# Kernel optimization log

Hardware: AMD Instinct MI355X
Metric: run time of the kernel (lower is better)

The kernel has to match this reference:

```python
import jax, jax.numpy as jnp
import numpy as np

# Dims: batch, in-ch, out-ch, deform kernel, channels-per-offset-group, input H/W
B, CIN, COUT, K, CPG, H, W = 16, 64, 64, 3, 8, 130, 130
G = CIN // CPG                 # number of deformable offset groups = 8
HO, WO = H - 2, W - 2          # conv1 (3x3, VALID) output == deform-conv output (3x3, VALID)
DN = ('NCHW', 'OIHW', 'NCHW')


def _conv(x, w, b):
    y = jax.lax.conv_general_dilated(x, w, (1, 1), 'VALID', dimension_numbers=DN)
    return y + b[None, :, None, None]


def setup_inputs() -> dict:
    key = jax.random.key(0)
    k0, k1, k2, k3 = jax.random.split(key, 4)
    def wn(k, shape, fan_in, scale=1.0):
        return jax.random.normal(k, shape, jnp.float32) * (scale / np.sqrt(fan_in))
    return {
        'x':  jax.random.normal(k0, (B, CIN, H, W), jnp.float32),
        'w1': wn(k1, (CIN, CIN, 3, 3), CIN * 9),
        'b1': jnp.zeros((CIN,), jnp.float32),
        # small scale so predicted offsets stay in a realistic sub-pixel/pixel range
        'w2': wn(k2, (G * 2 * K * K, CIN, 1, 1), CIN, scale=0.1),
        'b2': jnp.zeros((G * 2 * K * K,), jnp.float32),
        'wd': wn(k3, (COUT, CIN, K, K), CIN * K * K),
    }


def _deform_conv(x, off, wd):
    # x: [B,CIN,H,W], off: [B,G*2*K*K,HO,WO], wd: [COUT,CIN,K,K]
    Bq, Cin, Hx, Wx = x.shape
    offr = off.reshape(Bq, G, K, K, 2, HO, WO)     # (dy, dx) per group/kernel-pos/pixel
    xg = x.reshape(Bq, G, CPG, Hx * Wx)            # grouped input, flat spatial
    hh = jnp.arange(HO, dtype=x.dtype)[:, None]
    ww = jnp.arange(WO, dtype=x.dtype)[None, :]
    out = jnp.zeros((Bq, COUT, HO, WO), x.dtype)

    def gather(yi, xi, valid):
        # yi/xi: clipped int coords [B,G,HO,WO]; valid: 0/1 mask (zero padding outside)
        idx = (yi * Wx + xi).reshape(Bq, G, 1, HO * WO)
        v = jnp.take_along_axis(xg, jnp.broadcast_to(idx, (Bq, G, CPG, HO * WO)), axis=-1)
        return v.reshape(Bq, G, CPG, HO, WO) * valid[:, :, None, :, :]

    for i in range(K):
        for j in range(K):
            py = offr[:, :, i, j, 0] + (hh + i)    # [B,G,HO,WO] sample row (float)
            px = offr[:, :, i, j, 1] + (ww + j)    # [B,G,HO,WO] sample col (float)
            y0 = jnp.floor(py); x0 = jnp.floor(px)
            ly = py - y0;       lx = px - x0
            y0i = y0.astype(jnp.int32); x0i = x0.astype(jnp.int32)
            y1i = y0i + 1;              x1i = x0i + 1
            inb = lambda yi, xi: ((yi >= 0) & (yi < Hx) & (xi >= 0) & (xi < Wx)).astype(x.dtype)
            yc0 = jnp.clip(y0i, 0, Hx - 1); yc1 = jnp.clip(y1i, 0, Hx - 1)
            xc0 = jnp.clip(x0i, 0, Wx - 1); xc1 = jnp.clip(x1i, 0, Wx - 1)
            v = (((1 - ly) * (1 - lx))[:, :, None] * gather(yc0, xc0, inb(y0i, x0i))
               + ((1 - ly) * lx)[:, :, None]       * gather(yc0, xc1, inb(y0i, x1i))
               + (ly * (1 - lx))[:, :, None]       * gather(yc1, xc0, inb(y1i, x0i))
               + (ly * lx)[:, :, None]             * gather(yc1, xc1, inb(y1i, x1i)))
            # accumulate this kernel tap: v [B,G,CPG,HO,WO] x wd[:,:,i,j] [COUT,G,CPG]
            out = out + jnp.einsum('bgchw,ogc->bohw', v, wd[:, :, i, j].reshape(COUT, G, CPG))
    return out


def reference(x, w1, b1, w2, b2, wd):
    off = _conv(_conv(x, w1, b1), w2, b2)          # [B, G*2*K*K, HO, WO]
    y = _deform_conv(x, off, wd)                   # [B, COUT, HO, WO]
    return (y, off)
```

## Files before the change

### kernel.cpp

```cpp
#include <hip/hip_runtime.h>

typedef unsigned short u16;
typedef unsigned int u32;
typedef __attribute__((ext_vector_type(8))) short bfrag;
typedef __attribute__((ext_vector_type(4))) float ffrag;

constexpr int B_ = 16, CIN = 64, COUT = 64, G = 8, CPG = 8;
constexpr int H = 130, W = 130, HO = 128, WO = 128;
constexpr int OFFC = 144;
constexpr int PLANE_IN = H * W;
constexpr int PLANE_OUT = HO * WO;

constexpr size_t WB1_BYTE = 36864 * 4;
constexpr size_t WB2_BYTE = WB1_BYTE + 36864 * 2;
constexpr size_t XT_BYTE  = 262144;
constexpr size_t XT_SIZE  = (size_t)B_ * PLANE_IN * 64 * 2;

__device__ __forceinline__ u16 f2bf(float f) {
    union { u32 u; float f; } t; t.f = f;
    return (u16)((t.u + 0x7FFFu + ((t.u >> 16) & 1u)) >> 16);
}
__device__ __forceinline__ float bf2f(short h) {
    union { u32 u; float f; } t; t.u = ((u32)(u16)h) << 16;
    return t.f;
}

__global__ void prep_weights(const float* __restrict__ w1,
                             const float* __restrict__ wd,
                             const float* __restrict__ w2,
                             float* __restrict__ wsf) {
    u16* wdB = (u16*)wsf;
    u16* wB1 = (u16*)((char*)wsf + WB1_BYTE);
    u16* wB2 = (u16*)((char*)wsf + WB2_BYTE);
    int idx = blockIdx.x * 256 + threadIdx.x;
    if (idx < 36864) {
        int co = idx / 576, r = idx % 576;
        int t = r >> 6, ci = r & 63;
        wdB[idx] = f2bf(wd[(co * 64 + ci) * 9 + t]);
    } else if (idx < 73728) {
        int j = idx - 36864;
        int co = j / 576, r = j % 576;
        int t = r >> 6, ci = r & 63;
        wB1[j] = f2bf(w1[(co * 64 + ci) * 9 + t]);
    } else if (idx < 82944) {
        int j = idx - 73728;
        wB2[j] = f2bf(w2[j]);
    }
}

__global__ __launch_bounds__(256) void x_to_nhwc(const float* __restrict__ x,
                                                 u16* __restrict__ xt) {
    int p = blockIdx.x * 256 + threadIdx.x;
    if (p >= B_ * PLANE_IN) return;
    int b = p / PLANE_IN, pp = p % PLANE_IN;
    const float* xb = x + (size_t)b * CIN * PLANE_IN + pp;
    u16* dst = xt + (size_t)p * 64;
    #pragma unroll
    for (int oct = 0; oct < 8; ++oct) {
        union { u16 h[8]; uint4 q; } pk;
        #pragma unroll
        for (int j = 0; j < 8; ++j)
            pk.h[j] = f2bf(xb[(size_t)(oct * 8 + j) * PLANE_IN]);
        *(uint4*)(dst + oct * 8) = pk.q;
    }
}

union ConvSmem {
    char xsb[324 * 128];
    char hsb[4][64 * 128];
};
__device__ __forceinline__ int swz128(int row, int bytecol) {
    return row * 128 + (bytecol ^ ((row & 7) << 4));
}

template<bool XT>
__global__ __launch_bounds__(256) void conv12(const float* __restrict__ x,
                                              const u16* __restrict__ xt,
                                              const float* __restrict__ b1,
                                              const float* __restrict__ b2,
                                              const float* __restrict__ wsf,
                                              float* __restrict__ off_out) {
    __shared__ ConvSmem sm;
    const u16* wB1 = (const u16*)((const char*)wsf + WB1_BYTE);
    const u16* wB2 = (const u16*)((const char*)wsf + WB2_BYTE);
    const int b = blockIdx.z;
    const int y0 = blockIdx.y * 16, x0 = blockIdx.x * 16;
    const int tid = threadIdx.x;
    const int wave = tid >> 6, lane = tid & 63;
    const int n16 = lane & 15, quad = lane >> 4;

    if constexpr (XT) {
        const u16* xtb = xt + (size_t)b * PLANE_IN * 64;
        for (int idx = tid; idx < 324 * 8; idx += 256) {
            int p = idx >> 3, oct = idx & 7;
            *(bfrag*)(sm.xsb + swz128(p, oct * 16)) =
                *(const bfrag*)&xtb[((size_t)(y0 + p / 18) * W + x0 + p % 18) * 64 + oct * 8];
        }
    } else {
        const float* xb = x + (size_t)b * CIN * PLANE_IN;
        for (int idx = tid; idx < 324 * 64; idx += 256) {
            int ci = idx / 324, p = idx % 324;
            float v = xb[(size_t)ci * PLANE_IN + (y0 + p / 18) * W + (x0 + p % 18)];
            *(u16*)(sm.xsb + swz128(p, ci * 2)) = f2bf(v);
        }
    }
    __syncthreads();

    ffrag acc[4][4];
    #pragma unroll
    for (int nt = 0; nt < 4; ++nt) {
        float bv = b1[nt * 16 + n16];
        #pragma unroll
        for (int mt = 0; mt < 4; ++mt) acc[mt][nt] = ffrag{bv, bv, bv, bv};
    }

    #pragma unroll
    for (int s = 0; s < 18; ++s) {
        const int tap = s >> 1, cib = (s & 1) * 32;
        const int ti = tap / 3, tj = tap % 3;
        bfrag a[4], bb[4];
        #pragma unroll
        for (int mt = 0; mt < 4; ++mt) {
            int p = (wave * 4 + mt + ti) * 18 + n16 + tj;
            a[mt] = *(const bfrag*)(sm.xsb + swz128(p, cib * 2 + quad * 16));
        }
        #pragma unroll
        for (int nt = 0; nt < 4; ++nt)
            bb[nt] = *(const bfrag*)&wB1[(nt * 16 + n16) * 576 + tap * 64 + cib + quad * 8];
        #pragma unroll
        for (int mt = 0; mt < 4; ++mt)
            #pragma unroll
            for (int nt = 0; nt < 4; ++nt)
                acc[mt][nt] = __builtin_amdgcn_mfma_f32_16x16x32_bf16(
                    a[mt], bb[nt], acc[mt][nt], 0, 0, 0);
    }

    __syncthreads();

    #pragma unroll
    for (int mt = 0; mt < 4; ++mt)
        #pragma unroll
        for (int nt = 0; nt < 4; ++nt)
            #pragma unroll
            for (int r = 0; r < 4; ++r)
                *(u16*)(sm.hsb[wave] + swz128(mt * 16 + quad * 4 + r, (nt * 16 + n16) * 2))
                    = f2bf(acc[mt][nt][r]);
    __syncthreads();

    bfrag a2[4][2];
    #pragma unroll
    for (int mt = 0; mt < 4; ++mt)
        #pragma unroll
        for (int s2 = 0; s2 < 2; ++s2)
            a2[mt][s2] = *(const bfrag*)(sm.hsb[wave]
                        + swz128(mt * 16 + n16, s2 * 64 + quad * 16));

    float* offb = off_out + (size_t)b * OFFC * PLANE_OUT;
    #pragma unroll 1
    for (int nt2 = 0; nt2 < 9; ++nt2) {
        bfrag b2f[2];
        #pragma unroll
        for (int s2 = 0; s2 < 2; ++s2)
            b2f[s2] = *(const bfrag*)&wB2[(nt2 * 16 + n16) * 64 + s2 * 32 + quad * 8];
        float bv = b2[nt2 * 16 + n16];
        #pragma unroll
        for (int mt = 0; mt < 4; ++mt) {
            ffrag acc2 = ffrag{bv, bv, bv, bv};
            acc2 = __builtin_amdgcn_mfma_f32_16x16x32_bf16(a2[mt][0], b2f[0], acc2, 0, 0, 0);
            acc2 = __builtin_amdgcn_mfma_f32_16x16x32_bf16(a2[mt][1], b2f[1], acc2, 0, 0, 0);
            float* dst = offb + (size_t)(nt2 * 16 + n16) * PLANE_OUT
                       + (y0 + wave * 4 + mt) * WO + x0 + quad * 4;
            *(ffrag*)dst = acc2;
        }
    }
}

__device__ __forceinline__ bfrag interp1(bfrag q0, bfrag q1, bfrag q2, bfrag q3,
                                         float w0, float w1, float w2, float w3) {
    union { u16 h[8]; bfrag f; } pk;
    #pragma unroll
    for (int j = 0; j < 8; ++j) {
        float v = w0 * bf2f(q0[j]) + w1 * bf2f(q1[j])
                + w2 * bf2f(q2[j]) + w3 * bf2f(q3[j]);
        pk.h[j] = f2bf(v);
    }
    return pk.f;
}

constexpr int TR = 14, TC = 22, TILE_PX = TR * TC;

__device__ __forceinline__ bfrag lds_px(const char* xls, int p, int g) {
    return *(const bfrag*)(xls + p * 128 + ((g * 16) ^ ((p & 7) << 4)));
}

template<bool XT>
__global__ __launch_bounds__(256, 4) void deform_k(const float* __restrict__ x,
                                                   const u16* __restrict__ xt,
                                                   const float* __restrict__ wsf,
                                                   const float* __restrict__ off_in,
                                                   float* __restrict__ y_out) {
    __shared__ char xls[TILE_PX * 128];
    const u16* wdB = (const u16*)wsf;

    const int wg = blockIdx.x;
    const int swz = (wg & 7) * 256 + (wg >> 3);
    const int b = swz >> 7, sp = swz & 127;
    const int y0 = (sp >> 3) * 8, x0 = (sp & 7) * 16;
    const int ylo = y0 - 2, xlo = x0 - 2;

    const int tid = threadIdx.x;
    const int wave = tid >> 6, lane = tid & 63;
    const int n16 = lane & 15, quad = lane >> 4;
    const int wo = x0 + n16;

    const float* offbase = off_in + (size_t)b * OFFC * PLANE_OUT + x0 + n16;
    const u16* xtb = xt + (size_t)b * PLANE_IN * 64;
    const float* xb = x + (size_t)b * CIN * PLANE_IN;

    if constexpr (XT) {
        for (int idx = tid; idx < TILE_PX * 8; idx += 256) {
            int oct = idx & 7, pix = idx >> 3;
            int ty = pix / TC, tx = pix % TC;
            int iy = min(max(ylo + ty, 0), H - 1);
            int ix = min(max(xlo + tx, 0), W - 1);
            *(bfrag*)(xls + pix * 128 + ((oct * 16) ^ ((pix & 7) << 4)))
                = *(const bfrag*)&xtb[((size_t)(iy * W + ix)) * 64 + oct * 8];
        }
        __syncthreads();
    }

    ffrag acc[2][4];
    #pragma unroll
    for (int mt = 0; mt < 2; ++mt)
        #pragma unroll
        for (int nt = 0; nt < 4; ++nt) acc[mt][nt] = ffrag{0.f, 0.f, 0.f, 0.f};

    float pdy[4], pdx[4];
    #pragma unroll
    for (int tk = 0; tk < 4; ++tk) {
        const int mt = tk >> 1, g = quad + (tk & 1) * 4;
        const float* ob = offbase + (y0 + wave * 2 + mt) * WO
                        + (size_t)(g * 9 * 2) * PLANE_OUT;
        pdy[tk] = ob[0];
        pdx[tk] = ob[PLANE_OUT];
    }

    #pragma unroll 1
    for (int t = 0; t < 9; ++t) {
        const int ki = t / 3, kj = t % 3;

        float dyv[4], dxv[4];
        #pragma unroll
        for (int tk = 0; tk < 4; ++tk) { dyv[tk] = pdy[tk]; dxv[tk] = pdx[tk]; }

        if (t < 8) {
            #pragma unroll
            for (int tk = 0; tk < 4; ++tk) {
                const int mt = tk >> 1, g = quad + (tk & 1) * 4;
                const float* ob = offbase + (y0 + wave * 2 + mt) * WO
                                + (size_t)((g * 9 + t + 1) * 2) * PLANE_OUT;
                pdy[tk] = ob[0];
                pdx[tk] = ob[PLANE_OUT];
            }
        }

        #pragma unroll
        for (int half = 0; half < 2; ++half) {
            const int g = quad + half * 4;
            bfrag bw0 = *(const bfrag*)&wdB[(size_t)(0 * 16 + n16) * 576 + t * 64 + half * 32 + quad * 8];
            bfrag bw1 = *(const bfrag*)&wdB[(size_t)(1 * 16 + n16) * 576 + t * 64 + half * 32 + quad * 8];
            bfrag bw2 = *(const bfrag*)&wdB[(size_t)(2 * 16 + n16) * 576 + t * 64 + half * 32 + quad * 8];
            bfrag bw3 = *(const bfrag*)&wdB[(size_t)(3 * 16 + n16) * 576 + t * 64 + half * 32 + quad * 8];

            #pragma unroll
            for (int mt = 0; mt < 2; ++mt) {
                const int tk = mt * 2 + half;
                const int ho = y0 + wave * 2 + mt;
                float py = dyv[tk] + (float)(ho + ki);
                float px = dxv[tk] + (float)(wo + kj);
                float y0f = floorf(py), x0f = floorf(px);
                float ly = py - y0f, lx = px - x0f;
                int yi0 = (int)y0f, xi0 = (int)x0f;
                int yi1 = yi0 + 1, xi1 = xi0 + 1;
                float vy0 = (yi0 >= 0 && yi0 < H) ? 1.f : 0.f;
                float vy1 = (yi1 >= 0 && yi1 < H) ? 1.f : 0.f;
                float vx0 = (xi0 >= 0 && xi0 < W) ? 1.f : 0.f;
                float vx1 = (xi1 >= 0 && xi1 < W) ? 1.f : 0.f;
                float w00 = (1.f - ly) * (1.f - lx) * vy0 * vx0;
                float w01 = (1.f - ly) * lx         * vy0 * vx1;
                float w10 = ly * (1.f - lx)         * vy1 * vx0;
                float w11 = ly * lx                 * vy1 * vx1;
                int yc0 = min(max(yi0, 0), H - 1), yc1 = min(max(yi1, 0), H - 1);
                int xc0 = min(max(xi0, 0), W - 1), xc1 = min(max(xi1, 0), W - 1);

                bfrag q00, q01, q10, q11;
                if constexpr (XT) {
                    int ry0 = yc0 - ylo, ry1 = yc1 - ylo;
                    int rx0 = xc0 - xlo, rx1 = xc1 - xlo;
                    bool intile = ((u32)ry0 < TR) & ((u32)ry1 < TR)
                                & ((u32)rx0 < TC) & ((u32)rx1 < TC);
                    if (intile) {
                        q00 = lds_px(xls, ry0 * TC + rx0, g);
                        q01 = lds_px(xls, ry0 * TC + rx1, g);
                        q10 = lds_px(xls, ry1 * TC + rx0, g);
                        q11 = lds_px(xls, ry1 * TC + rx1, g);
                    } else {
                        q00 = *(const bfrag*)&xtb[(size_t)(yc0 * W + xc0) * 64 + g * 8];
                        q01 = *(const bfrag*)&xtb[(size_t)(yc0 * W + xc1) * 64 + g * 8];
                        q10 = *(const bfrag*)&xtb[(size_t)(yc1 * W + xc0) * 64 + g * 8];
                        q11 = *(const bfrag*)&xtb[(size_t)(yc1 * W + xc1) * 64 + g * 8];
                    }
                } else {
                    int i00 = yc0 * W + xc0, i01 = yc0 * W + xc1;
                    int i10 = yc1 * W + xc0, i11 = yc1 * W + xc1;
                    const float* xg = xb + (size_t)g * CPG * PLANE_IN;
                    union { u16 h[8]; bfrag f; } p00, p01, p10, p11;
                    #pragma unroll
                    for (int cc = 0; cc < 8; ++cc) {
                        const float* xp = xg + cc * PLANE_IN;
                        p00.h[cc] = f2bf(xp[i00]); p01.h[cc] = f2bf(xp[i01]);
                        p10.h[cc] = f2bf(xp[i10]); p11.h[cc] = f2bf(xp[i11]);
                    }
                    q00 = p00.f; q01 = p01.f; q10 = p10.f; q11 = p11.f;
                }

                bfrag fr = interp1(q00, q01, q10, q11, w00, w01, w10, w11);

                acc[mt][0] = __builtin_amdgcn_mfma_f32_16x16x32_bf16(fr, bw0, acc[mt][0], 0, 0, 0);
                acc[mt][1] = __builtin_amdgcn_mfma_f32_16x16x32_bf16(fr, bw1, acc[mt][1], 0, 0, 0);
                acc[mt][2] = __builtin_amdgcn_mfma_f32_16x16x32_bf16(fr, bw2, acc[mt][2], 0, 0, 0);
                acc[mt][3] = __builtin_amdgcn_mfma_f32_16x16x32_bf16(fr, bw3, acc[mt][3], 0, 0, 0);
            }
        }
    }

    float* yb = y_out + (size_t)b * COUT * PLANE_OUT;
    #pragma unroll
    for (int nt = 0; nt < 4; ++nt)
        #pragma unroll
        for (int mt = 0; mt < 2; ++mt) {
            float* dst = yb + (size_t)(nt * 16 + n16) * PLANE_OUT
                       + (y0 + wave * 2 + mt) * WO + x0 + quad * 4;
            *(ffrag*)dst = acc[mt][nt];
        }
}

extern "C" void kernel_launch(void* const* d_in, const int* in_sizes, int n_in,
                              void* d_out, int out_size, void* d_ws, size_t ws_size,
                              hipStream_t stream) {
    const float* x  = (const float*)d_in[0];
    const float* w1 = (const float*)d_in[1];
    const float* b1 = (const float*)d_in[2];
    const float* w2 = (const float*)d_in[3];
    const float* b2 = (const float*)d_in[4];
    const float* wd = (const float*)d_in[5];
    float* y_out = (float*)d_out;
    float* off_out = y_out + (size_t)B_ * COUT * PLANE_OUT;
    float* wsf = (float*)d_ws;
    u16* xt = (u16*)((char*)d_ws + XT_BYTE);
    const bool use_xt = ws_size >= XT_BYTE + XT_SIZE;

    prep_weights<<<324, 256, 0, stream>>>(w1, wd, w2, wsf);
    if (use_xt) {
        x_to_nhwc<<<(B_ * PLANE_IN + 255) / 256, 256, 0, stream>>>(x, xt);
        conv12<true><<<dim3(8, 8, B_), 256, 0, stream>>>(x, xt, b1, b2, wsf, off_out);
        deform_k<true><<<2048, 256, 0, stream>>>(x, xt, wsf, off_out, y_out);
    } else {
        conv12<false><<<dim3(8, 8, B_), 256, 0, stream>>>(x, xt, b1, b2, wsf, off_out);
        deform_k<false><<<2048, 256, 0, stream>>>(x, xt, wsf, off_out, y_out);
    }
}
```

Before: 431.4 us.

## Prefetch conv weights one step ahead and shrink deform input halo tile

In conv12, the first-stage and second-stage weight fragments are now loaded one iteration ahead in registers. The main K loop is no longer unrolled, and the kernel gets a launch-bounds occupancy hint. In deform_k, the staged input tile shrinks from a 2-pixel halo to a 1-pixel halo, which cuts LDS per block, and the occupancy hint rises to 5 blocks per CU. This trades possible extra fallback gathers for samples that land outside the smaller tile, and looser unrolling, for more resident waves and hidden weight-load latency.

```diff
diff --git a/kernel.cpp b/kernel.cpp
--- a/kernel.cpp
+++ b/kernel.cpp
@@ -74,12 +74,12 @@
 }
 
 template<bool XT>
-__global__ __launch_bounds__(256) void conv12(const float* __restrict__ x,
-                                              const u16* __restrict__ xt,
-                                              const float* __restrict__ b1,
-                                              const float* __restrict__ b2,
-                                              const float* __restrict__ wsf,
-                                              float* __restrict__ off_out) {
+__global__ __launch_bounds__(256, 3) void conv12(const float* __restrict__ x,
+                                                 const u16* __restrict__ xt,
+                                                 const float* __restrict__ b1,
+                                                 const float* __restrict__ b2,
+                                                 const float* __restrict__ wsf,
+                                                 float* __restrict__ off_out) {
     __shared__ ConvSmem sm;
     const u16* wB1 = (const u16*)((const char*)wsf + WB1_BYTE);
     const u16* wB2 = (const u16*)((const char*)wsf + WB2_BYTE);
@@ -114,25 +114,37 @@
         for (int mt = 0; mt < 4; ++mt) acc[mt][nt] = ffrag{bv, bv, bv, bv};
     }
 
-    #pragma unroll
+    bfrag nb0 = *(const bfrag*)&wB1[(0 * 16 + n16) * 576 + quad * 8];
+    bfrag nb1 = *(const bfrag*)&wB1[(1 * 16 + n16) * 576 + quad * 8];
+    bfrag nb2 = *(const bfrag*)&wB1[(2 * 16 + n16) * 576 + quad * 8];
+    bfrag nb3 = *(const bfrag*)&wB1[(3 * 16 + n16) * 576 + quad * 8];
+
+    #pragma unroll 1
     for (int s = 0; s < 18; ++s) {
         const int tap = s >> 1, cib = (s & 1) * 32;
         const int ti = tap / 3, tj = tap % 3;
-        bfrag a[4], bb[4];
+        bfrag bb0 = nb0, bb1 = nb1, bb2 = nb2, bb3 = nb3;
+        if (s < 17) {
+            const int s2 = s + 1;
+            const int koff = (s2 >> 1) * 64 + (s2 & 1) * 32 + quad * 8;
+            nb0 = *(const bfrag*)&wB1[(0 * 16 + n16) * 576 + koff];
+            nb1 = *(const bfrag*)&wB1[(1 * 16 + n16) * 576 + koff];
+            nb2 = *(const bfrag*)&wB1[(2 * 16 + n16) * 576 + koff];
+            nb3 = *(const bfrag*)&wB1[(3 * 16 + n16) * 576 + koff];
+        }
+        bfrag a[4];
         #pragma unroll
         for (int mt = 0; mt < 4; ++mt) {
             int p = (wave * 4 + mt + ti) * 18 + n16 + tj;
             a[mt] = *(const bfrag*)(sm.xsb + swz128(p, cib * 2 + quad * 16));
         }
         #pragma unroll
-        for (int nt = 0; nt < 4; ++nt)
-            bb[nt] = *(const bfrag*)&wB1[(nt * 16 + n16) * 576 + tap * 64 + cib + quad * 8];
-        #pragma unroll
-        for (int mt = 0; mt < 4; ++mt)
-            #pragma unroll
-            for (int nt = 0; nt < 4; ++nt)
-                acc[mt][nt] = __builtin_amdgcn_mfma_f32_16x16x32_bf16(
-                    a[mt], bb[nt], acc[mt][nt], 0, 0, 0);
+        for (int mt = 0; mt < 4; ++mt) {
+            acc[mt][0] = __builtin_amdgcn_mfma_f32_16x16x32_bf16(a[mt], bb0, acc[mt][0], 0, 0, 0);
+            acc[mt][1] = __builtin_amdgcn_mfma_f32_16x16x32_bf16(a[mt], bb1, acc[mt][1], 0, 0, 0);
+            acc[mt][2] = __builtin_amdgcn_mfma_f32_16x16x32_bf16(a[mt], bb2, acc[mt][2], 0, 0, 0);
+            acc[mt][3] = __builtin_amdgcn_mfma_f32_16x16x32_bf16(a[mt], bb3, acc[mt][3], 0, 0, 0);
+        }
     }
 
     __syncthreads();
@@ -156,18 +168,22 @@
                         + swz128(mt * 16 + n16, s2 * 64 + quad * 16));
 
     float* offb = off_out + (size_t)b * OFFC * PLANE_OUT;
+    bfrag c0n = *(const bfrag*)&wB2[(size_t)n16 * 64 + quad * 8];
+    bfrag c1n = *(const bfrag*)&wB2[(size_t)n16 * 64 + 32 + quad * 8];
     #pragma unroll 1
     for (int nt2 = 0; nt2 < 9; ++nt2) {
-        bfrag b2f[2];
-        #pragma unroll
-        for (int s2 = 0; s2 < 2; ++s2)
-            b2f[s2] = *(const bfrag*)&wB2[(nt2 * 16 + n16) * 64 + s2 * 32 + quad * 8];
+        bfrag b2f0 = c0n, b2f1 = c1n;
+        if (nt2 < 8) {
+            const u16* wp = &wB2[(size_t)((nt2 + 1) * 16 + n16) * 64 + quad * 8];
+            c0n = *(const bfrag*)wp;
+            c1n = *(const bfrag*)(wp + 32);
+        }
         float bv = b2[nt2 * 16 + n16];
         #pragma unroll
         for (int mt = 0; mt < 4; ++mt) {
             ffrag acc2 = ffrag{bv, bv, bv, bv};
-            acc2 = __builtin_amdgcn_mfma_f32_16x16x32_bf16(a2[mt][0], b2f[0], acc2, 0, 0, 0);
-            acc2 = __builtin_amdgcn_mfma_f32_16x16x32_bf16(a2[mt][1], b2f[1], acc2, 0, 0, 0);
+            acc2 = __builtin_amdgcn_mfma_f32_16x16x32_bf16(a2[mt][0], b2f0, acc2, 0, 0, 0);
+            acc2 = __builtin_amdgcn_mfma_f32_16x16x32_bf16(a2[mt][1], b2f1, acc2, 0, 0, 0);
             float* dst = offb + (size_t)(nt2 * 16 + n16) * PLANE_OUT
                        + (y0 + wave * 4 + mt) * WO + x0 + quad * 4;
             *(ffrag*)dst = acc2;
@@ -187,14 +203,14 @@
     return pk.f;
 }
 
-constexpr int TR = 14, TC = 22, TILE_PX = TR * TC;
+constexpr int TR = 12, TC = 20, TILE_PX = TR * TC;
 
 __device__ __forceinline__ bfrag lds_px(const char* xls, int p, int g) {
     return *(const bfrag*)(xls + p * 128 + ((g * 16) ^ ((p & 7) << 4)));
 }
 
 template<bool XT>
-__global__ __launch_bounds__(256, 4) void deform_k(const float* __restrict__ x,
+__global__ __launch_bounds__(256, 5) void deform_k(const float* __restrict__ x,
                                                    const u16* __restrict__ xt,
                                                    const float* __restrict__ wsf,
                                                    const float* __restrict__ off_in,
@@ -206,7 +222,7 @@
     const int swz = (wg & 7) * 256 + (wg >> 3);
     const int b = swz >> 7, sp = swz & 127;
     const int y0 = (sp >> 3) * 8, x0 = (sp & 7) * 16;
-    const int ylo = y0 - 2, xlo = x0 - 2;
+    const int ylo = y0 - 1, xlo = x0 - 1;
 
     const int tid = threadIdx.x;
     const int wave = tid >> 6, lane = tid & 63;
```

Result: slower. 583.4 us (+35.2%).

## Fuse offset convolutions and deformable conv into one kernel per tile

Applied to the files above, without the earlier changes.

Merges the conv1+conv2 offset kernel and the deformable conv kernel into a single fused kernel over 16x16 tiles. It loads a 20x20 halo tile of NHWC bf16 input into LDS once and reuses it for both the 3x3 conv and the bilinear gathers. Offsets are written to global and read back in the same block, removing one launch and the duplicated tile load. The cost is far fewer blocks (1024 vs 2048), a larger per-thread register footprint with launch bounds lowered to 2, and a per-row barrier loop in the second conv stage. The fallback non-NHWC path is kept as separate simplified kernels.

```diff
diff --git a/kernel.cpp b/kernel.cpp
--- a/kernel.cpp
+++ b/kernel.cpp
@@ -65,44 +65,53 @@
     }
 }
 
-union ConvSmem {
-    char xsb[324 * 128];
-    char hsb[4][64 * 128];
-};
 __device__ __forceinline__ int swz128(int row, int bytecol) {
     return row * 128 + (bytecol ^ ((row & 7) << 4));
 }
-
-template<bool XT>
-__global__ __launch_bounds__(256) void conv12(const float* __restrict__ x,
-                                              const u16* __restrict__ xt,
-                                              const float* __restrict__ b1,
-                                              const float* __restrict__ b2,
-                                              const float* __restrict__ wsf,
-                                              float* __restrict__ off_out) {
-    __shared__ ConvSmem sm;
+__device__ __forceinline__ bfrag lds_px(const char* xls, int p, int g) {
+    return *(const bfrag*)(xls + p * 128 + ((g * 16) ^ ((p & 7) << 4)));
+}
+__device__ __forceinline__ bfrag interp1(bfrag q0, bfrag q1, bfrag q2, bfrag q3,
+                                         float w0, float w1, float w2, float w3) {
+    union { u16 h[8]; bfrag f; } pk;
+    #pragma unroll
+    for (int j = 0; j < 8; ++j) {
+        float v = w0 * bf2f(q0[j]) + w1 * bf2f(q1[j])
+                + w2 * bf2f(q2[j]) + w3 * bf2f(q3[j]);
+        pk.h[j] = f2bf(v);
+    }
+    return pk.f;
+}
+
+constexpr int FTR = 20, FTC = 20, FT_PX = FTR * FTC;
+
+__global__ __launch_bounds__(256, 2) void fused_cd(const u16* __restrict__ xt,
+                                                   const float* __restrict__ b1,
+                                                   const float* __restrict__ b2,
+                                                   const float* __restrict__ wsf,
+                                                   float* __restrict__ off_out,
+                                                   float* __restrict__ y_out) {
+    __shared__ char xls[FT_PX * 128];
+    __shared__ char hsl[4][16 * 128];
+    const u16* wdB = (const u16*)wsf;
     const u16* wB1 = (const u16*)((const char*)wsf + WB1_BYTE);
     const u16* wB2 = (const u16*)((const char*)wsf + WB2_BYTE);
+
     const int b = blockIdx.z;
     const int y0 = blockIdx.y * 16, x0 = blockIdx.x * 16;
+    const int ylo = y0 - 1, xlo = x0 - 1;
     const int tid = threadIdx.x;
     const int wave = tid >> 6, lane = tid & 63;
     const int n16 = lane & 15, quad = lane >> 4;
-
-    if constexpr (XT) {
-        const u16* xtb = xt + (size_t)b * PLANE_IN * 64;
-        for (int idx = tid; idx < 324 * 8; idx += 256) {
-            int p = idx >> 3, oct = idx & 7;
-            *(bfrag*)(sm.xsb + swz128(p, oct * 16)) =
-                *(const bfrag*)&xtb[((size_t)(y0 + p / 18) * W + x0 + p % 18) * 64 + oct * 8];
-        }
-    } else {
-        const float* xb = x + (size_t)b * CIN * PLANE_IN;
-        for (int idx = tid; idx < 324 * 64; idx += 256) {
-            int ci = idx / 324, p = idx % 324;
-            float v = xb[(size_t)ci * PLANE_IN + (y0 + p / 18) * W + (x0 + p % 18)];
-            *(u16*)(sm.xsb + swz128(p, ci * 2)) = f2bf(v);
-        }
+    const u16* xtb = xt + (size_t)b * PLANE_IN * 64;
+
+    for (int idx = tid; idx < FT_PX * 8; idx += 256) {
+        int oct = idx & 7, pix = idx >> 3;
+        int ty = pix / FTC, tx = pix % FTC;
+        int iy = min(max(ylo + ty, 0), H - 1);
+        int ix = min(max(xlo + tx, 0), W - 1);
+        *(bfrag*)(xls + pix * 128 + ((oct * 16) ^ ((pix & 7) << 4)))
+            = *(const bfrag*)&xtb[((size_t)(iy * W + ix)) * 64 + oct * 8];
     }
     __syncthreads();
 
@@ -113,7 +122,6 @@
         #pragma unroll
         for (int mt = 0; mt < 4; ++mt) acc[mt][nt] = ffrag{bv, bv, bv, bv};
     }
-
     #pragma unroll
     for (int s = 0; s < 18; ++s) {
         const int tap = s >> 1, cib = (s & 1) * 32;
@@ -121,8 +129,8 @@
         bfrag a[4], bb[4];
         #pragma unroll
         for (int mt = 0; mt < 4; ++mt) {
-            int p = (wave * 4 + mt + ti) * 18 + n16 + tj;
-            a[mt] = *(const bfrag*)(sm.xsb + swz128(p, cib * 2 + quad * 16));
+            int p = (wave * 4 + mt + ti + 1) * FTC + (n16 + tj + 1);
+            a[mt] = *(const bfrag*)(xls + swz128(p, cib * 2 + quad * 16));
         }
         #pragma unroll
         for (int nt = 0; nt < 4; ++nt)
@@ -135,149 +143,72 @@
                     a[mt], bb[nt], acc[mt][nt], 0, 0, 0);
     }
 
-    __syncthreads();
-
-    #pragma unroll
-    for (int mt = 0; mt < 4; ++mt)
-        #pragma unroll
-        for (int nt = 0; nt < 4; ++nt)
-            #pragma unroll
-            for (int r = 0; r < 4; ++r)
-                *(u16*)(sm.hsb[wave] + swz128(mt * 16 + quad * 4 + r, (nt * 16 + n16) * 2))
-                    = f2bf(acc[mt][nt][r]);
-    __syncthreads();
-
-    bfrag a2[4][2];
-    #pragma unroll
-    for (int mt = 0; mt < 4; ++mt)
-        #pragma unroll
-        for (int s2 = 0; s2 < 2; ++s2)
-            a2[mt][s2] = *(const bfrag*)(sm.hsb[wave]
-                        + swz128(mt * 16 + n16, s2 * 64 + quad * 16));
-
     float* offb = off_out + (size_t)b * OFFC * PLANE_OUT;
     #pragma unroll 1
-    for (int nt2 = 0; nt2 < 9; ++nt2) {
-        bfrag b2f[2];
-        #pragma unroll
-        for (int s2 = 0; s2 < 2; ++s2)
-            b2f[s2] = *(const bfrag*)&wB2[(nt2 * 16 + n16) * 64 + s2 * 32 + quad * 8];
-        float bv = b2[nt2 * 16 + n16];
-        #pragma unroll
-        for (int mt = 0; mt < 4; ++mt) {
+    for (int mt = 0; mt < 4; ++mt) {
+        #pragma unroll
+        for (int nt = 0; nt < 4; ++nt)
+            #pragma unroll
+            for (int r = 0; r < 4; ++r)
+                *(u16*)(hsl[wave] + swz128(quad * 4 + r, (nt * 16 + n16) * 2))
+                    = f2bf(acc[mt][nt][r]);
+        __syncthreads();
+        bfrag a20 = *(const bfrag*)(hsl[wave] + swz128(n16, quad * 16));
+        bfrag a21 = *(const bfrag*)(hsl[wave] + swz128(n16, 64 + quad * 16));
+        #pragma unroll 1
+        for (int nt2 = 0; nt2 < 9; ++nt2) {
+            const u16* wp = &wB2[(size_t)(nt2 * 16 + n16) * 64 + quad * 8];
+            bfrag b2f0 = *(const bfrag*)wp;
+            bfrag b2f1 = *(const bfrag*)(wp + 32);
+            float bv = b2[nt2 * 16 + n16];
             ffrag acc2 = ffrag{bv, bv, bv, bv};
-            acc2 = __builtin_amdgcn_mfma_f32_16x16x32_bf16(a2[mt][0], b2f[0], acc2, 0, 0, 0);
-            acc2 = __builtin_amdgcn_mfma_f32_16x16x32_bf16(a2[mt][1], b2f[1], acc2, 0, 0, 0);
+            acc2 = __builtin_amdgcn_mfma_f32_16x16x32_bf16(a20, b2f0, acc2, 0, 0, 0);
+            acc2 = __builtin_amdgcn_mfma_f32_16x16x32_bf16(a21, b2f1, acc2, 0, 0, 0);
             float* dst = offb + (size_t)(nt2 * 16 + n16) * PLANE_OUT
                        + (y0 + wave * 4 + mt) * WO + x0 + quad * 4;
             *(ffrag*)dst = acc2;
         }
-    }
-}
-
-__device__ __forceinline__ bfrag interp1(bfrag q0, bfrag q1, bfrag q2, bfrag q3,
-                                         float w0, float w1, float w2, float w3) {
-    union { u16 h[8]; bfrag f; } pk;
-    #pragma unroll
-    for (int j = 0; j < 8; ++j) {
-        float v = w0 * bf2f(q0[j]) + w1 * bf2f(q1[j])
-                + w2 * bf2f(q2[j]) + w3 * bf2f(q3[j]);
-        pk.h[j] = f2bf(v);
-    }
-    return pk.f;
-}
-
-constexpr int TR = 14, TC = 22, TILE_PX = TR * TC;
-
-__device__ __forceinline__ bfrag lds_px(const char* xls, int p, int g) {
-    return *(const bfrag*)(xls + p * 128 + ((g * 16) ^ ((p & 7) << 4)));
-}
-
-template<bool XT>
-__global__ __launch_bounds__(256, 4) void deform_k(const float* __restrict__ x,
-                                                   const u16* __restrict__ xt,
-                                                   const float* __restrict__ wsf,
-                                                   const float* __restrict__ off_in,
-                                                   float* __restrict__ y_out) {
-    __shared__ char xls[TILE_PX * 128];
-    const u16* wdB = (const u16*)wsf;
-
-    const int wg = blockIdx.x;
-    const int swz = (wg & 7) * 256 + (wg >> 3);
-    const int b = swz >> 7, sp = swz & 127;
-    const int y0 = (sp >> 3) * 8, x0 = (sp & 7) * 16;
-    const int ylo = y0 - 2, xlo = x0 - 2;
-
-    const int tid = threadIdx.x;
-    const int wave = tid >> 6, lane = tid & 63;
-    const int n16 = lane & 15, quad = lane >> 4;
+        __syncthreads();
+    }
+
     const int wo = x0 + n16;
-
-    const float* offbase = off_in + (size_t)b * OFFC * PLANE_OUT + x0 + n16;
-    const u16* xtb = xt + (size_t)b * PLANE_IN * 64;
-    const float* xb = x + (size_t)b * CIN * PLANE_IN;
-
-    if constexpr (XT) {
-        for (int idx = tid; idx < TILE_PX * 8; idx += 256) {
-            int oct = idx & 7, pix = idx >> 3;
-            int ty = pix / TC, tx = pix % TC;
-            int iy = min(max(ylo + ty, 0), H - 1);
-            int ix = min(max(xlo + tx, 0), W - 1);
-            *(bfrag*)(xls + pix * 128 + ((oct * 16) ^ ((pix & 7) << 4)))
-                = *(const bfrag*)&xtb[((size_t)(iy * W + ix)) * 64 + oct * 8];
-        }
-        __syncthreads();
-    }
-
-    ffrag acc[2][4];
-    #pragma unroll
-    for (int mt = 0; mt < 2; ++mt)
-        #pragma unroll
-        for (int nt = 0; nt < 4; ++nt) acc[mt][nt] = ffrag{0.f, 0.f, 0.f, 0.f};
-
-    float pdy[4], pdx[4];
-    #pragma unroll
-    for (int tk = 0; tk < 4; ++tk) {
-        const int mt = tk >> 1, g = quad + (tk & 1) * 4;
-        const float* ob = offbase + (y0 + wave * 2 + mt) * WO
-                        + (size_t)(g * 9 * 2) * PLANE_OUT;
-        pdy[tk] = ob[0];
-        pdx[tk] = ob[PLANE_OUT];
-    }
+    ffrag accd[4][4];
+    #pragma unroll
+    for (int mt = 0; mt < 4; ++mt)
+        #pragma unroll
+        for (int nt = 0; nt < 4; ++nt) accd[mt][nt] = ffrag{0.f, 0.f, 0.f, 0.f};
 
     #pragma unroll 1
-    for (int t = 0; t < 9; ++t) {
-        const int ki = t / 3, kj = t % 3;
-
-        float dyv[4], dxv[4];
-        #pragma unroll
-        for (int tk = 0; tk < 4; ++tk) { dyv[tk] = pdy[tk]; dxv[tk] = pdx[tk]; }
-
-        if (t < 8) {
-            #pragma unroll
-            for (int tk = 0; tk < 4; ++tk) {
-                const int mt = tk >> 1, g = quad + (tk & 1) * 4;
-                const float* ob = offbase + (y0 + wave * 2 + mt) * WO
-                                + (size_t)((g * 9 + t + 1) * 2) * PLANE_OUT;
-                pdy[tk] = ob[0];
-                pdx[tk] = ob[PLANE_OUT];
+    for (int mt = 0; mt < 4; ++mt) {
+        const int ho = y0 + wave * 4 + mt;
+        const float* ob = offb + ho * WO + x0 + n16;
+        float pdy0 = ob[(size_t)((quad * 9) * 2 + 0) * PLANE_OUT];
+        float pdx0 = ob[(size_t)((quad * 9) * 2 + 1) * PLANE_OUT];
+        float pdy1 = ob[(size_t)(((quad + 4) * 9) * 2 + 0) * PLANE_OUT];
+        float pdx1 = ob[(size_t)(((quad + 4) * 9) * 2 + 1) * PLANE_OUT];
+
+        #pragma unroll 1
+        for (int t = 0; t < 9; ++t) {
+            const int ki = t / 3, kj = t % 3;
+            float dy0 = pdy0, dx0 = pdx0, dy1 = pdy1, dx1 = pdx1;
+            if (t < 8) {
+                pdy0 = ob[(size_t)((quad * 9 + t + 1) * 2 + 0) * PLANE_OUT];
+                pdx0 = ob[(size_t)((quad * 9 + t + 1) * 2 + 1) * PLANE_OUT];
+                pdy1 = ob[(size_t)(((quad + 4) * 9 + t + 1) * 2 + 0) * PLANE_OUT];
+                pdx1 = ob[(size_t)(((quad + 4) * 9 + t + 1) * 2 + 1) * PLANE_OUT];
             }
-        }
-
-        #pragma unroll
-        for (int half = 0; half < 2; ++half) {
-            const int g = quad + half * 4;
-            bfrag bw0 = *(const bfrag*)&wdB[(size_t)(0 * 16 + n16) * 576 + t * 64 + half * 32 + quad * 8];
-            bfrag bw1 = *(const bfrag*)&wdB[(size_t)(1 * 16 + n16) * 576 + t * 64 + half * 32 + quad * 8];
-            bfrag bw2 = *(const bfrag*)&wdB[(size_t)(2 * 16 + n16) * 576 + t * 64 + half * 32 + quad * 8];
-            bfrag bw3 = *(const bfrag*)&wdB[(size_t)(3 * 16 + n16) * 576 + t * 64 + half * 32 + quad * 8];
-
-            #pragma unroll
-            for (int mt = 0; mt < 2; ++mt) {
-                const int tk = mt * 2 + half;
-                const int ho = y0 + wave * 2 + mt;
-                float py = dyv[tk] + (float)(ho + ki);
-                float px = dxv[tk] + (float)(wo + kj);
+            #pragma unroll
+            for (int half = 0; half < 2; ++half) {
+                const int g = quad + half * 4;
+                const float dyv = half ? dy1 : dy0;
+                const float dxv = half ? dx1 : dx0;
+                bfrag bw0 = *(const bfrag*)&wdB[(size_t)(0 * 16 + n16) * 576 + t * 64 + half * 32 + quad * 8];
+                bfrag bw1 = *(const bfrag*)&wdB[(size_t)(1 * 16 + n16) * 576 + t * 64 + half * 32 + quad * 8];
+                bfrag bw2 = *(const bfrag*)&wdB[(size_t)(2 * 16 + n16) * 576 + t * 64 + half * 32 + quad * 8];
+                bfrag bw3 = *(const bfrag*)&wdB[(size_t)(3 * 16 + n16) * 576 + t * 64 + half * 32 + quad * 8];
+
+                float py = dyv + (float)(ho + ki);
+                float px = dxv + (float)(wo + kj);
                 float y0f = floorf(py), x0f = floorf(px);
                 float ly = py - y0f, lx = px - x0f;
                 int yi0 = (int)y0f, xi0 = (int)x0f;
@@ -293,39 +224,197 @@
                 int yc0 = min(max(yi0, 0), H - 1), yc1 = min(max(yi1, 0), H - 1);
                 int xc0 = min(max(xi0, 0), W - 1), xc1 = min(max(xi1, 0), W - 1);
 
+                int ry0 = yc0 - ylo, ry1 = yc1 - ylo;
+                int rx0 = xc0 - xlo, rx1 = xc1 - xlo;
+                bool intile = ((u32)ry0 < FTR) & ((u32)ry1 < FTR)
+                            & ((u32)rx0 < FTC) & ((u32)rx1 < FTC);
                 bfrag q00, q01, q10, q11;
-                if constexpr (XT) {
-                    int ry0 = yc0 - ylo, ry1 = yc1 - ylo;
-                    int rx0 = xc0 - xlo, rx1 = xc1 - xlo;
-                    bool intile = ((u32)ry0 < TR) & ((u32)ry1 < TR)
-                                & ((u32)rx0 < TC) & ((u32)rx1 < TC);
-                    if (intile) {
-                        q00 = lds_px(xls, ry0 * TC + rx0, g);
-                        q01 = lds_px(xls, ry0 * TC + rx1, g);
-                        q10 = lds_px(xls, ry1 * TC + rx0, g);
-                        q11 = lds_px(xls, ry1 * TC + rx1, g);
-                    } else {
-                        q00 = *(const bfrag*)&xtb[(size_t)(yc0 * W + xc0) * 64 + g * 8];
-                        q01 = *(const bfrag*)&xtb[(size_t)(yc0 * W + xc1) * 64 + g * 8];
-                        q10 = *(const bfrag*)&xtb[(size_t)(yc1 * W + xc0) * 64 + g * 8];
-                        q11 = *(const bfrag*)&xtb[(size_t)(yc1 * W + xc1) * 64 + g * 8];
-                    }
+                if (intile) {
+                    q00 = lds_px(xls, ry0 * FTC + rx0, g);
+                    q01 = lds_px(xls, ry0 * FTC + rx1, g);
+                    q10 = lds_px(xls, ry1 * FTC + rx0, g);
+                    q11 = lds_px(xls, ry1 * FTC + rx1, g);
                 } else {
-                    int i00 = yc0 * W + xc0, i01 = yc0 * W + xc1;
-                    int i10 = yc1 * W + xc0, i11 = yc1 * W + xc1;
-                    const float* xg = xb + (size_t)g * CPG * PLANE_IN;
-                    union { u16 h[8]; bfrag f; } p00, p01, p10, p11;
-                    #pragma unroll
-                    for (int cc = 0; cc < 8; ++cc) {
-                        const float* xp = xg + cc * PLANE_IN;
-                        p00.h[cc] = f2bf(xp[i00]); p01.h[cc] = f2bf(xp[i01]);
-                        p10.h[cc] = f2bf(xp[i10]); p11.h[cc] = f2bf(xp[i11]);
-                    }
-                    q00 = p00.f; q01 = p01.f; q10 = p10.f; q11 = p11.f;
+                    q00 = *(const bfrag*)&xtb[(size_t)(yc0 * W + xc0) * 64 + g * 8];
+                    q01 = *(const bfrag*)&xtb[(size_t)(yc0 * W + xc1) * 64 + g * 8];
+                    q10 = *(const bfrag*)&xtb[(size_t)(yc1 * W + xc0) * 64 + g * 8];
+                    q11 = *(const bfrag*)&xtb[(size_t)(yc1 * W + xc1) * 64 + g * 8];
                 }
-
                 bfrag fr = interp1(q00, q01, q10, q11, w00, w01, w10, w11);
 
+                accd[mt][0] = __builtin_amdgcn_mfma_f32_16x16x32_bf16(fr, bw0, accd[mt][0], 0, 0, 0);
+                accd[mt][1] = __builtin_amdgcn_mfma_f32_16x16x32_bf16(fr, bw1, accd[mt][1], 0, 0, 0);
+                accd[mt][2] = __builtin_amdgcn_mfma_f32_16x16x32_bf16(fr, bw2, accd[mt][2], 0, 0, 0);
+                accd[mt][3] = __builtin_amdgcn_mfma_f32_16x16x32_bf16(fr, bw3, accd[mt][3], 0, 0, 0);
+            }
+        }
+    }
+
+    float* yb = y_out + (size_t)b * COUT * PLANE_OUT;
+    #pragma unroll
+    for (int nt = 0; nt < 4; ++nt)
+        #pragma unroll
+        for (int mt = 0; mt < 4; ++mt) {
+            float* dst = yb + (size_t)(nt * 16 + n16) * PLANE_OUT
+                       + (y0 + wave * 4 + mt) * WO + x0 + quad * 4;
+            *(ffrag*)dst = accd[mt][nt];
+        }
+}
+
+union ConvSmem {
+    char xsb[324 * 128];
+    char hsb[4][64 * 128];
+};
+
+__global__ __launch_bounds__(256) void conv12_f(const float* __restrict__ x,
+                                                const float* __restrict__ b1,
+                                                const float* __restrict__ b2,
+                                                const float* __restrict__ wsf,
+                                                float* __restrict__ off_out) {
+    __shared__ ConvSmem sm;
+    const u16* wB1 = (const u16*)((const char*)wsf + WB1_BYTE);
+    const u16* wB2 = (const u16*)((const char*)wsf + WB2_BYTE);
+    const int b = blockIdx.z;
+    const int y0 = blockIdx.y * 16, x0 = blockIdx.x * 16;
+    const int tid = threadIdx.x;
+    const int wave = tid >> 6, lane = tid & 63;
+    const int n16 = lane & 15, quad = lane >> 4;
+
+    const float* xb = x + (size_t)b * CIN * PLANE_IN;
+    for (int idx = tid; idx < 324 * 64; idx += 256) {
+        int ci = idx / 324, p = idx % 324;
+        float v = xb[(size_t)ci * PLANE_IN + (y0 + p / 18) * W + (x0 + p % 18)];
+        *(u16*)(sm.xsb + swz128(p, ci * 2)) = f2bf(v);
+    }
+    __syncthreads();
+
+    ffrag acc[4][4];
+    #pragma unroll
+    for (int nt = 0; nt < 4; ++nt) {
+        float bv = b1[nt * 16 + n16];
+        #pragma unroll
+        for (int mt = 0; mt < 4; ++mt) acc[mt][nt] = ffrag{bv, bv, bv, bv};
+    }
+    #pragma unroll
+    for (int s = 0; s < 18; ++s) {
+        const int tap = s >> 1, cib = (s & 1) * 32;
+        const int ti = tap / 3, tj = tap % 3;
+        bfrag a[4], bb[4];
+        #pragma unroll
+        for (int mt = 0; mt < 4; ++mt) {
+            int p = (wave * 4 + mt + ti) * 18 + n16 + tj;
+            a[mt] = *(const bfrag*)(sm.xsb + swz128(p, cib * 2 + quad * 16));
+        }
+        #pragma unroll
+        for (int nt = 0; nt < 4; ++nt)
+            bb[nt] = *(const bfrag*)&wB1[(nt * 16 + n16) * 576 + tap * 64 + cib + quad * 8];
+        #pragma unroll
+        for (int mt = 0; mt < 4; ++mt)
+            #pragma unroll
+            for (int nt = 0; nt < 4; ++nt)
+                acc[mt][nt] = __builtin_amdgcn_mfma_f32_16x16x32_bf16(
+                    a[mt], bb[nt], acc[mt][nt], 0, 0, 0);
+    }
+    __syncthreads();
+    #pragma unroll
+    for (int mt = 0; mt < 4; ++mt)
+        #pragma unroll
+        for (int nt = 0; nt < 4; ++nt)
+            #pragma unroll
+            for (int r = 0; r < 4; ++r)
+                *(u16*)(sm.hsb[wave] + swz128(mt * 16 + quad * 4 + r, (nt * 16 + n16) * 2))
+                    = f2bf(acc[mt][nt][r]);
+    __syncthreads();
+    bfrag a2[4][2];
+    #pragma unroll
+    for (int mt = 0; mt < 4; ++mt)
+        #pragma unroll
+        for (int s2 = 0; s2 < 2; ++s2)
+            a2[mt][s2] = *(const bfrag*)(sm.hsb[wave]
+                        + swz128(mt * 16 + n16, s2 * 64 + quad * 16));
+    float* offb = off_out + (size_t)b * OFFC * PLANE_OUT;
+    #pragma unroll 1
+    for (int nt2 = 0; nt2 < 9; ++nt2) {
+        const u16* wp = &wB2[(size_t)(nt2 * 16 + n16) * 64 + quad * 8];
+        bfrag b2f0 = *(const bfrag*)wp;
+        bfrag b2f1 = *(const bfrag*)(wp + 32);
+        float bv = b2[nt2 * 16 + n16];
+        #pragma unroll
+        for (int mt = 0; mt < 4; ++mt) {
+            ffrag acc2 = ffrag{bv, bv, bv, bv};
+            acc2 = __builtin_amdgcn_mfma_f32_16x16x32_bf16(a2[mt][0], b2f0, acc2, 0, 0, 0);
+            acc2 = __builtin_amdgcn_mfma_f32_16x16x32_bf16(a2[mt][1], b2f1, acc2, 0, 0, 0);
+            float* dst = offb + (size_t)(nt2 * 16 + n16) * PLANE_OUT
+                       + (y0 + wave * 4 + mt) * WO + x0 + quad * 4;
+            *(ffrag*)dst = acc2;
+        }
+    }
+}
+
+__global__ __launch_bounds__(256, 4) void deform_f(const float* __restrict__ x,
+                                                   const float* __restrict__ wsf,
+                                                   const float* __restrict__ off_in,
+                                                   float* __restrict__ y_out) {
+    const u16* wdB = (const u16*)wsf;
+    const int wg = blockIdx.x;
+    const int swz = (wg & 7) * 256 + (wg >> 3);
+    const int b = swz >> 7, sp = swz & 127;
+    const int y0 = (sp >> 3) * 8, x0 = (sp & 7) * 16;
+    const int tid = threadIdx.x;
+    const int wave = tid >> 6, lane = tid & 63;
+    const int n16 = lane & 15, quad = lane >> 4;
+    const int wo = x0 + n16;
+    const float* offbase = off_in + (size_t)b * OFFC * PLANE_OUT + x0 + n16;
+    const float* xb = x + (size_t)b * CIN * PLANE_IN;
+
+    ffrag acc[2][4];
+    #pragma unroll
+    for (int mt = 0; mt < 2; ++mt)
+        #pragma unroll
+        for (int nt = 0; nt < 4; ++nt) acc[mt][nt] = ffrag{0.f, 0.f, 0.f, 0.f};
+
+    #pragma unroll 1
+    for (int t = 0; t < 9; ++t) {
+        const int ki = t / 3, kj = t % 3;
+        #pragma unroll
+        for (int half = 0; half < 2; ++half) {
+            const int g = quad + half * 4;
+            bfrag bw0 = *(const bfrag*)&wdB[(size_t)(0 * 16 + n16) * 576 + t * 64 + half * 32 + quad * 8];
+            bfrag bw1 = *(const bfrag*)&wdB[(size_t)(1 * 16 + n16) * 576 + t * 64 + half * 32 + quad * 8];
+            bfrag bw2 = *(const bfrag*)&wdB[(size_t)(2 * 16 + n16) * 576 + t * 64 + half * 32 + quad * 8];
+            bfrag bw3 = *(const bfrag*)&wdB[(size_t)(3 * 16 + n16) * 576 + t * 64 + half * 32 + quad * 8];
+            #pragma unroll
+            for (int mt = 0; mt < 2; ++mt) {
+                const int ho = y0 + wave * 2 + mt;
+                const float* ob = offbase + ho * WO + (size_t)((g * 9 + t) * 2) * PLANE_OUT;
+                float py = ob[0] + (float)(ho + ki);
+                float px = ob[PLANE_OUT] + (float)(wo + kj);
+                float y0f = floorf(py), x0f = floorf(px);
+                float ly = py - y0f, lx = px - x0f;
+                int yi0 = (int)y0f, xi0 = (int)x0f;
+                int yi1 = yi0 + 1, xi1 = xi0 + 1;
+                float vy0 = (yi0 >= 0 && yi0 < H) ? 1.f : 0.f;
+                float vy1 = (yi1 >= 0 && yi1 < H) ? 1.f : 0.f;
+                float vx0 = (xi0 >= 0 && xi0 < W) ? 1.f : 0.f;
+                float vx1 = (xi1 >= 0 && xi1 < W) ? 1.f : 0.f;
+                float w00 = (1.f - ly) * (1.f - lx) * vy0 * vx0;
+                float w01 = (1.f - ly) * lx         * vy0 * vx1;
+                float w10 = ly * (1.f - lx)         * vy1 * vx0;
+                float w11 = ly * lx                 * vy1 * vx1;
+                int yc0 = min(max(yi0, 0), H - 1), yc1 = min(max(yi1, 0), H - 1);
+                int xc0 = min(max(xi0, 0), W - 1), xc1 = min(max(xi1, 0), W - 1);
+                int i00 = yc0 * W + xc0, i01 = yc0 * W + xc1;
+                int i10 = yc1 * W + xc0, i11 = yc1 * W + xc1;
+                const float* xg = xb + (size_t)g * CPG * PLANE_IN;
+                union { u16 h[8]; bfrag f; } pk;
+                #pragma unroll
+                for (int cc = 0; cc < 8; ++cc) {
+                    const float* xp = xg + cc * PLANE_IN;
+                    float v = w00 * xp[i00] + w01 * xp[i01]
+                            + w10 * xp[i10] + w11 * xp[i11];
+                    pk.h[cc] = f2bf(v);
+                }
+                bfrag fr = pk.f;
                 acc[mt][0] = __builtin_amdgcn_mfma_f32_16x16x32_bf16(fr, bw0, acc[mt][0], 0, 0, 0);
                 acc[mt][1] = __builtin_amdgcn_mfma_f32_16x16x32_bf16(fr, bw1, acc[mt][1], 0, 0, 0);
                 acc[mt][2] = __builtin_amdgcn_mfma_f32_16x16x32_bf16(fr, bw2, acc[mt][2], 0, 0, 0);
@@ -333,7 +422,6 @@
             }
         }
     }
-
     float* yb = y_out + (size_t)b * COUT * PLANE_OUT;
     #pragma unroll
     for (int nt = 0; nt < 4; ++nt)
@@ -363,10 +451,9 @@
     prep_weights<<<324, 256, 0, stream>>>(w1, wd, w2, wsf);
     if (use_xt) {
         x_to_nhwc<<<(B_ * PLANE_IN + 255) / 256, 256, 0, stream>>>(x, xt);
-        conv12<true><<<dim3(8, 8, B_), 256, 0, stream>>>(x, xt, b1, b2, wsf, off_out);
-        deform_k<true><<<2048, 256, 0, stream>>>(x, xt, wsf, off_out, y_out);
+        fused_cd<<<dim3(8, 8, B_), 256, 0, stream>>>(xt, b1, b2, wsf, off_out, y_out);
     } else {
-        conv12<false><<<dim3(8, 8, B_), 256, 0, stream>>>(x, xt, b1, b2, wsf, off_out);
-        deform_k<false><<<2048, 256, 0, stream>>>(x, xt, wsf, off_out, y_out);
-    }
-}
+        conv12_f<<<dim3(8, 8, B_), 256, 0, stream>>>(x, b1, b2, wsf, off_out);
+        deform_f<<<2048, 256, 0, stream>>>(x, wsf, off_out, y_out);
+    }
+}
```

Measured after the change: 545.4 us. 1.26x slower.
